# Optimization experiments

Measured on AMD Instinct MI355X. Metric: run time of the kernel, lower is better.

The kernel has to match this reference:

```python
import jax, jax.numpy as jnp
import numpy as np

B, S, E, H = 4, 2048, 1024, 16
D = E // H  # head dim = 64


def setup_inputs() -> dict:
    key = jax.random.key(0)
    ks = jax.random.split(key, 5)
    s = 0.02
    return {
        "x": jax.random.normal(ks[0], (B, S, E), dtype=jnp.float32),
        "Wq": jax.random.normal(ks[1], (E, E), dtype=jnp.float32) * s,
        "Wk": jax.random.normal(ks[2], (E, E), dtype=jnp.float32) * s,
        "Wv": jax.random.normal(ks[3], (E, E), dtype=jnp.float32) * s,
        "Wo": jax.random.normal(ks[4], (E, E), dtype=jnp.float32) * s,
        "bo": jnp.zeros((E,), dtype=jnp.float32),
    }


def reference(x, Wq, Wk, Wv, Wo, bo):
    b, s, e = x.shape
    h, d = H, e // H
    # QKV projections -> [b, h, s, d]
    q = (x @ Wq).reshape(b, s, h, d).transpose(0, 2, 1, 3)
    k = (x @ Wk).reshape(b, s, h, d).transpose(0, 2, 1, 3)
    v = (x @ Wv).reshape(b, s, h, d).transpose(0, 2, 1, 3)
    # scores [b, h, s, s], causal mask with -inf, scaled softmax
    a = jnp.einsum('bhqd,bhkd->bhqk', q, k)
    causal = jnp.tril(jnp.ones((s, s), dtype=bool))  # True where allowed
    a = jnp.where(causal, a, -jnp.inf) / jnp.sqrt(jnp.asarray(d, x.dtype))
    a = jax.nn.softmax(a, axis=-1)
    # dropout p=0.0 (identity in eval)
    y = jnp.einsum('bhqk,bhkd->bhqd', a, v)
    y = y.transpose(0, 2, 1, 3).reshape(b, s, e)
    return y @ Wo + bo
```

## Files before the change

kernel.cpp:

```cpp
#include <hip/hip_runtime.h>

typedef __bf16 bf16x8 __attribute__((ext_vector_type(8)));
typedef float f32x4 __attribute__((ext_vector_type(4)));
typedef unsigned short u16x8 __attribute__((ext_vector_type(8)));

#define S_LEN 2048
#define NHEAD 16
#define HDIM  64
#define EMB   1024

__device__ __forceinline__ ushort f2b(float v) {
  union { float f; unsigned u; } x; x.f = v;
  unsigned r = (x.u + 0x7fffu + ((x.u >> 16) & 1u)) >> 16;
  return (ushort)r;
}

__device__ __forceinline__ unsigned packtrunc(float a, float b) {
  union { float f; unsigned u; } x, y; x.f = a; y.f = b;
  return (x.u >> 16) | (y.u & 0xFFFF0000u);
}

typedef const __attribute__((address_space(1))) unsigned int* gp1_t;
typedef __attribute__((address_space(3))) unsigned int* lp3_t;
__device__ __forceinline__ void gld16(const ushort* g, const ushort* l) {
  __builtin_amdgcn_global_load_lds((gp1_t)(unsigned long long)(uintptr_t)g,
                                   (lp3_t)(unsigned int)(uintptr_t)l, 16, 0, 0);
}

__global__ __launch_bounds__(256) void prep_kernel(
    const float* __restrict__ x, const float* __restrict__ W0,
    const float* __restrict__ W1, const float* __restrict__ W2,
    const float* __restrict__ W3, ushort* __restrict__ xb,
    ushort* __restrict__ Wt0, ushort* __restrict__ Wt1,
    ushort* __restrict__ Wt2, ushort* __restrict__ Wt3, float scale0) {
  const int z = blockIdx.z;
  if (z == 4) {
    size_t base = ((size_t)(blockIdx.y * 32 + blockIdx.x)) * 8192 + threadIdx.x * 4;
#pragma unroll
    for (int i = 0; i < 8; ++i) {
      float4 v = *(const float4*)(x + base + i * 1024);
      ushort4 o;
      o.x = f2b(v.x); o.y = f2b(v.y); o.z = f2b(v.z); o.w = f2b(v.w);
      *(ushort4*)(xb + base + i * 1024) = o;
    }
    return;
  }
  __shared__ float t[32][33];
  const float* W = z == 0 ? W0 : (z == 1 ? W1 : (z == 2 ? W2 : W3));
  ushort* Wt = z == 0 ? Wt0 : (z == 1 ? Wt1 : (z == 2 ? Wt2 : Wt3));
  const float scale = z == 0 ? scale0 : 1.0f;
  int k0 = blockIdx.x * 32, n0 = blockIdx.y * 32;
  int c = threadIdx.x & 31, r0 = threadIdx.x >> 5;
#pragma unroll
  for (int i = 0; i < 4; ++i) {
    int r = r0 + i * 8;
    t[r][c] = W[(size_t)(k0 + r) * EMB + n0 + c];
  }
  __syncthreads();
#pragma unroll
  for (int i = 0; i < 4; ++i) {
    int r = r0 + i * 8;
    Wt[(size_t)(n0 + r) * EMB + k0 + c] = f2b(t[c][r] * scale);
  }
}

template <int EPI>
__global__ __launch_bounds__(256) void gemm_kernel(
    const ushort* __restrict__ A, const ushort* __restrict__ Bt, int K, int N,
    ushort* __restrict__ outQ, ushort* __restrict__ outK, ushort* __restrict__ outVt,
    float* __restrict__ outF, const float* __restrict__ bias) {
  __shared__ ushort As[2][128 * 32];
  __shared__ ushort Bs[2][128 * 32];
  const int tid = threadIdx.x;
  const int lane = tid & 63, ln = lane & 15, quad = lane >> 4;
  const int wave = tid >> 6, wm = wave >> 1, wn = wave & 1;
  const long m0 = (long)blockIdx.x * 128, n0 = (long)blockIdx.y * 128;

  const int sr = lane >> 2, sc = (lane & 3) * 8;
  const ushort* AgL = A + (m0 + 32 * wave + sr) * (long)K + sc;
  const ushort* BgL = Bt + (n0 + 32 * wave + sr) * (long)K + sc;

  f32x4 acc[4][4] = {};
  const int KT = K >> 5;

  {
    ushort* as = &As[0][32 * wave * 32];
    ushort* bs = &Bs[0][32 * wave * 32];
    gld16(AgL, as);
    gld16(AgL + 16 * (long)K, as + 16 * 32);
    gld16(BgL, bs);
    gld16(BgL + 16 * (long)K, bs + 16 * 32);
  }
  __syncthreads();

  for (int kt = 0; kt < KT; ++kt) {
    if (kt + 1 < KT) {
      const int nb = (kt + 1) & 1;
      const ushort* a = AgL + (kt + 1) * 32;
      const ushort* b = BgL + (kt + 1) * 32;
      ushort* as = &As[nb][32 * wave * 32];
      ushort* bs = &Bs[nb][32 * wave * 32];
      gld16(a, as);
      gld16(a + 16 * (long)K, as + 16 * 32);
      gld16(b, bs);
      gld16(b + 16 * (long)K, bs + 16 * 32);
    }
    const ushort* Ac = &As[kt & 1][0];
    const ushort* Bc = &Bs[kt & 1][0];
    bf16x8 af[4], bf[4];
#pragma unroll
    for (int mt = 0; mt < 4; ++mt)
      af[mt] = *(const bf16x8*)(Ac + (wm * 64 + mt * 16 + ln) * 32 + quad * 8);
#pragma unroll
    for (int nt = 0; nt < 4; ++nt)
      bf[nt] = *(const bf16x8*)(Bc + (wn * 64 + nt * 16 + ln) * 32 + quad * 8);
#pragma unroll
    for (int mt = 0; mt < 4; ++mt)
#pragma unroll
      for (int nt = 0; nt < 4; ++nt)
        acc[mt][nt] = __builtin_amdgcn_mfma_f32_16x16x32_bf16(af[mt], bf[nt], acc[mt][nt], 0, 0, 0);
    __syncthreads();
  }

  if (EPI == 0) {
    const int sel = (int)(n0 >> 10);
    if (sel == 2) {
#pragma unroll
      for (int mt = 0; mt < 4; ++mt) {
        const long mbase = m0 + wm * 64 + mt * 16 + quad * 4;
        const long bb = mbase >> 11, s = mbase & 2047;
#pragma unroll
        for (int nt = 0; nt < 4; ++nt) {
          const int nn = (int)((n0 & 1023) + wn * 64 + nt * 16 + ln);
          const int h = nn >> 6, d = nn & 63;
          uint2 val;
          val.x = (unsigned)f2b(acc[mt][nt][0]) | ((unsigned)f2b(acc[mt][nt][1]) << 16);
          val.y = (unsigned)f2b(acc[mt][nt][2]) | ((unsigned)f2b(acc[mt][nt][3]) << 16);
          *(uint2*)(outVt + (((bb * NHEAD + h) * (long)HDIM + d) * S_LEN) + s) = val;
        }
      }
    } else {
      ushort* dst = sel == 0 ? outQ : outK;
#pragma unroll
      for (int mt = 0; mt < 4; ++mt) {
#pragma unroll
        for (int nt = 0; nt < 4; ++nt) {
          const int nn = (int)((n0 & 1023) + wn * 64 + nt * 16 + ln);
          const int h = nn >> 6, d = nn & 63;
#pragma unroll
          for (int r = 0; r < 4; ++r) {
            const long m = m0 + wm * 64 + mt * 16 + quad * 4 + r;
            const long bb = m >> 11, s = m & 2047;
            dst[(((bb * NHEAD + h) * S_LEN) + s) * HDIM + d] = f2b(acc[mt][nt][r]);
          }
        }
      }
    }
  } else {
#pragma unroll
    for (int mt = 0; mt < 4; ++mt) {
#pragma unroll
      for (int nt = 0; nt < 4; ++nt) {
#pragma unroll
        for (int r = 0; r < 4; ++r) {
          const long m = m0 + wm * 64 + mt * 16 + quad * 4 + r;
          const long n = n0 + wn * 64 + nt * 16 + ln;
          outF[m * (long)N + n] = acc[mt][nt][r] + bias[n];
        }
      }
    }
  }
}

__global__ __launch_bounds__(256) void attn_kernel(const ushort* __restrict__ Q,
                                                   const ushort* __restrict__ Kg,
                                                   const ushort* __restrict__ Vt,
                                                   ushort* __restrict__ Y) {
  __shared__ alignas(16) ushort Ks[2][2 * 64 * 32];
  __shared__ alignas(16) ushort Vs[2][2 * 64 * 32];
  __shared__ alignas(16) ushort Ps[4 * 2 * 16 * 72];
  const int tid = threadIdx.x;
  const int wave = tid >> 6, lane = tid & 63, ln = lane & 15, quad = lane >> 4;
  const int bh = blockIdx.x;
  const int qb = 15 - (int)blockIdx.y;
  const int q0 = qb * 128;
  const size_t base = (size_t)bh * S_LEN * HDIM;
  const int ntiles = 2 * qb + 2;
  const int qbase = q0 + wave * 32;

  const u16x8 ob = {0x3F80, 0x3F80, 0x3F80, 0x3F80, 0x3F80, 0x3F80, 0x3F80, 0x3F80};
  const bf16x8 ones = __builtin_bit_cast(bf16x8, ob);

  bf16x8 qf[2][2];
#pragma unroll
  for (int mt = 0; mt < 2; ++mt)
#pragma unroll
    for (int ks2 = 0; ks2 < 2; ++ks2)
      qf[mt][ks2] = *(const bf16x8*)(Q + base + (size_t)(qbase + mt * 16 + ln) * HDIM +
                                     ks2 * 32 + quad * 8);

  f32x4 acc[2][4] = {};
  f32x4 accl[2] = {};

  const int sr = lane >> 2, sc = (lane & 3) * 8;
  const ushort* KgL = Kg + base + (size_t)(16 * wave + sr) * HDIM + sc;
  const ushort* VgL = Vt + base + (size_t)(16 * wave + sr) * S_LEN + sc;

  {
    ushort* kb = &Ks[0][16 * wave * 32];
    ushort* vb = &Vs[0][16 * wave * 32];
    gld16(KgL, kb);
    gld16(KgL + 32, kb + 2048);
    gld16(VgL, vb);
    gld16(VgL + 32, vb + 2048);
  }
  __syncthreads();

  ushort* Pw0 = Ps + wave * 2304;
  ushort* Pw1 = Pw0 + 1152;

  for (int kt = 0; kt < ntiles; ++kt) {
    const int cur = kt & 1;
    const int k0 = kt * 64;
    if (kt + 1 < ntiles) {
      const int nb = cur ^ 1;
      const size_t k1 = (size_t)(k0 + 64);
      ushort* kb = &Ks[nb][16 * wave * 32];
      ushort* vb = &Vs[nb][16 * wave * 32];
      gld16(KgL + k1 * HDIM, kb);
      gld16(KgL + k1 * HDIM + 32, kb + 2048);
      gld16(VgL + k1, vb);
      gld16(VgL + k1 + 32, vb + 2048);
    }
    const ushort* Kc = &Ks[cur][0];
    const ushort* Vc = &Vs[cur][0];

    if (k0 < qbase + 32) {
      f32x4 sT0[4] = {}, sT1[4] = {};
#pragma unroll
      for (int ks2 = 0; ks2 < 2; ++ks2) {
#pragma unroll
        for (int nt = 0; nt < 4; ++nt) {
          bf16x8 ak = *(const bf16x8*)(Kc + ks2 * 2048 + (nt * 16 + ln) * 32 + quad * 8);
          sT0[nt] = __builtin_amdgcn_mfma_f32_16x16x32_bf16(ak, qf[0][ks2], sT0[nt], 0, 0, 0);
          sT1[nt] = __builtin_amdgcn_mfma_f32_16x16x32_bf16(ak, qf[1][ks2], sT1[nt], 0, 0, 0);
        }
      }

      if (k0 + 63 > qbase) {
        const int thr0 = qbase + ln - k0 - quad * 4;
        const int thr1 = thr0 + 16;
#pragma unroll
        for (int nt = 0; nt < 4; ++nt)
#pragma unroll
          for (int r = 0; r < 4; ++r) {
            if (nt * 16 + r > thr0) sT0[nt][r] = -3.0e38f;
            if (nt * 16 + r > thr1) sT1[nt][r] = -3.0e38f;
          }
      }

      asm volatile("" ::: "memory");
#pragma unroll
      for (int nt = 0; nt < 4; ++nt) {
        uint2 w0, w1;
        w0.x = packtrunc(__builtin_amdgcn_exp2f(sT0[nt][0]), __builtin_amdgcn_exp2f(sT0[nt][1]));
        w0.y = packtrunc(__builtin_amdgcn_exp2f(sT0[nt][2]), __builtin_amdgcn_exp2f(sT0[nt][3]));
        w1.x = packtrunc(__builtin_amdgcn_exp2f(sT1[nt][0]), __builtin_amdgcn_exp2f(sT1[nt][1]));
        w1.y = packtrunc(__builtin_amdgcn_exp2f(sT1[nt][2]), __builtin_amdgcn_exp2f(sT1[nt][3]));
        const int off = ln * 72 + nt * 16 + quad * 4;
        *(uint2*)(Pw0 + off) = w0;
        *(uint2*)(Pw1 + off) = w1;
      }
      asm volatile("" ::: "memory");

#pragma unroll
      for (int ks2 = 0; ks2 < 2; ++ks2) {
        const int rcol = ks2 * 32 + quad * 8;
        bf16x8 ap0 = *(const bf16x8*)(Pw0 + ln * 72 + rcol);
        bf16x8 ap1 = *(const bf16x8*)(Pw1 + ln * 72 + rcol);
        accl[0] = __builtin_amdgcn_mfma_f32_16x16x32_bf16(ap0, ones, accl[0], 0, 0, 0);
        accl[1] = __builtin_amdgcn_mfma_f32_16x16x32_bf16(ap1, ones, accl[1], 0, 0, 0);
#pragma unroll
        for (int t2 = 0; t2 < 4; ++t2) {
          bf16x8 bv = *(const bf16x8*)(Vc + ks2 * 2048 + (t2 * 16 + ln) * 32 + quad * 8);
          acc[0][t2] = __builtin_amdgcn_mfma_f32_16x16x32_bf16(ap0, bv, acc[0][t2], 0, 0, 0);
          acc[1][t2] = __builtin_amdgcn_mfma_f32_16x16x32_bf16(ap1, bv, acc[1][t2], 0, 0, 0);
        }
      }
    }
    __syncthreads();
  }

  const long b = bh >> 4;
  const int h = bh & 15;
#pragma unroll
  for (int mt = 0; mt < 2; ++mt) {
#pragma unroll
    for (int r = 0; r < 4; ++r) {
      float inv = 1.0f / accl[mt][r];
      const int qq = qbase + mt * 16 + quad * 4 + r;
#pragma unroll
      for (int t2 = 0; t2 < 4; ++t2)
        Y[(((b * S_LEN + qq) * NHEAD) + h) * HDIM + t2 * 16 + ln] = f2b(acc[mt][t2][r] * inv);
    }
  }
}

extern "C" void kernel_launch(void* const* d_in, const int* in_sizes, int n_in,
                              void* d_out, int out_size, void* d_ws, size_t ws_size,
                              hipStream_t stream) {
  const float* x  = (const float*)d_in[0];
  const float* Wq = (const float*)d_in[1];
  const float* Wk = (const float*)d_in[2];
  const float* Wv = (const float*)d_in[3];
  const float* Wo = (const float*)d_in[4];
  const float* bo = (const float*)d_in[5];
  float* out = (float*)d_out;

  const size_t XE = (size_t)8192 * EMB;
  ushort* ws    = (ushort*)d_ws;
  ushort* xb    = ws;
  ushort* Wtqkv = xb + XE;
  ushort* Wto   = Wtqkv + 3 * 1048576;
  ushort* Qb    = Wto + 1048576;
  ushort* Kb    = Qb + XE;
  ushort* Vtb   = Kb + XE;
  ushort* Yb    = xb;

  const float SCALE_Q = 1.4426950408889634f / 8.0f;

  prep_kernel<<<dim3(32, 32, 5), 256, 0, stream>>>(
      x, Wq, Wk, Wv, Wo, xb, Wtqkv, Wtqkv + 1048576, Wtqkv + 2097152, Wto, SCALE_Q);

  gemm_kernel<0><<<dim3(64, 24), 256, 0, stream>>>(xb, Wtqkv, EMB, 3072,
                                                   Qb, Kb, Vtb, nullptr, nullptr);
  attn_kernel<<<dim3(64, 16), 256, 0, stream>>>(Qb, Kb, Vtb, Yb);
  gemm_kernel<1><<<dim3(64, 8), 256, 0, stream>>>(Yb, Wto, EMB, EMB,
                                                  nullptr, nullptr, nullptr, out, bo);
}
```

Measured before the change: 241.9 us.

## Double attention query tile per block to 256 rows for K/V reuse

Each attention block now handles 256 query rows (64 per wave, four 16-row sub-tiles) instead of 128, which halves the grid and doubles reuse of each staged K/V tile. K and V fragments are loaded into registers once per tile and shared across the four sub-tiles, and fully masked sub-tiles are skipped. Block order is rearranged so the heavy causal tiles are interleaved with light ones. The cost is more registers per wave (launch bounds set to 2 blocks), a larger P buffer in shared memory, and fewer blocks for load balancing.

```diff
diff --git a/kernel.cpp b/kernel.cpp
--- a/kernel.cpp
+++ b/kernel.cpp
@@ -172,35 +172,36 @@
   }
 }
 
-__global__ __launch_bounds__(256) void attn_kernel(const ushort* __restrict__ Q,
-                                                   const ushort* __restrict__ Kg,
-                                                   const ushort* __restrict__ Vt,
-                                                   ushort* __restrict__ Y) {
+__global__ __launch_bounds__(256, 2) void attn_kernel(const ushort* __restrict__ Q,
+                                                      const ushort* __restrict__ Kg,
+                                                      const ushort* __restrict__ Vt,
+                                                      ushort* __restrict__ Y) {
   __shared__ alignas(16) ushort Ks[2][2 * 64 * 32];
   __shared__ alignas(16) ushort Vs[2][2 * 64 * 32];
-  __shared__ alignas(16) ushort Ps[4 * 2 * 16 * 72];
+  __shared__ alignas(16) ushort Ps[4 * 4 * 16 * 72];
   const int tid = threadIdx.x;
   const int wave = tid >> 6, lane = tid & 63, ln = lane & 15, quad = lane >> 4;
   const int bh = blockIdx.x;
-  const int qb = 15 - (int)blockIdx.y;
-  const int q0 = qb * 128;
+  const int yb = (int)blockIdx.y;
+  const int qb = yb < 4 ? 7 - yb : yb - 4;
+  const int q0 = qb * 256;
   const size_t base = (size_t)bh * S_LEN * HDIM;
-  const int ntiles = 2 * qb + 2;
-  const int qbase = q0 + wave * 32;
+  const int ntiles = 4 * qb + 4;
+  const int qbase = q0 + wave * 64;
 
   const u16x8 ob = {0x3F80, 0x3F80, 0x3F80, 0x3F80, 0x3F80, 0x3F80, 0x3F80, 0x3F80};
   const bf16x8 ones = __builtin_bit_cast(bf16x8, ob);
 
-  bf16x8 qf[2][2];
-#pragma unroll
-  for (int mt = 0; mt < 2; ++mt)
+  bf16x8 qf[4][2];
+#pragma unroll
+  for (int h = 0; h < 4; ++h)
 #pragma unroll
     for (int ks2 = 0; ks2 < 2; ++ks2)
-      qf[mt][ks2] = *(const bf16x8*)(Q + base + (size_t)(qbase + mt * 16 + ln) * HDIM +
-                                     ks2 * 32 + quad * 8);
-
-  f32x4 acc[2][4] = {};
-  f32x4 accl[2] = {};
+      qf[h][ks2] = *(const bf16x8*)(Q + base + (size_t)(qbase + h * 16 + ln) * HDIM +
+                                    ks2 * 32 + quad * 8);
+
+  f32x4 acc[4][4] = {};
+  f32x4 accl[4] = {};
 
   const int sr = lane >> 2, sc = (lane & 3) * 8;
   const ushort* KgL = Kg + base + (size_t)(16 * wave + sr) * HDIM + sc;
@@ -216,8 +217,7 @@
   }
   __syncthreads();
 
-  ushort* Pw0 = Ps + wave * 2304;
-  ushort* Pw1 = Pw0 + 1152;
+  ushort* Pw = Ps + wave * 4608;
 
   for (int kt = 0; kt < ntiles; ++kt) {
     const int cur = kt & 1;
@@ -235,56 +235,61 @@
     const ushort* Kc = &Ks[cur][0];
     const ushort* Vc = &Vs[cur][0];
 
-    if (k0 < qbase + 32) {
-      f32x4 sT0[4] = {}, sT1[4] = {};
-#pragma unroll
-      for (int ks2 = 0; ks2 < 2; ++ks2) {
+    if (k0 < qbase + 64) {
+      bf16x8 ak[2][4];
+#pragma unroll
+      for (int ks2 = 0; ks2 < 2; ++ks2)
+#pragma unroll
+        for (int nt = 0; nt < 4; ++nt)
+          ak[ks2][nt] = *(const bf16x8*)(Kc + ks2 * 2048 + (nt * 16 + ln) * 32 + quad * 8);
+
+      asm volatile("" ::: "memory");
+#pragma unroll
+      for (int h = 0; h < 4; ++h) {
+        if (k0 > qbase + h * 16 + 15) continue;
+        f32x4 sT[4] = {};
+#pragma unroll
+        for (int ks2 = 0; ks2 < 2; ++ks2)
+#pragma unroll
+          for (int nt = 0; nt < 4; ++nt)
+            sT[nt] = __builtin_amdgcn_mfma_f32_16x16x32_bf16(ak[ks2][nt], qf[h][ks2], sT[nt], 0, 0, 0);
+
+        if (k0 + 63 > qbase + h * 16) {
+          const int thr = qbase + h * 16 + ln - k0 - quad * 4;
+#pragma unroll
+          for (int nt = 0; nt < 4; ++nt)
+#pragma unroll
+            for (int r = 0; r < 4; ++r)
+              if (nt * 16 + r > thr) sT[nt][r] = -3.0e38f;
+        }
+
 #pragma unroll
         for (int nt = 0; nt < 4; ++nt) {
-          bf16x8 ak = *(const bf16x8*)(Kc + ks2 * 2048 + (nt * 16 + ln) * 32 + quad * 8);
-          sT0[nt] = __builtin_amdgcn_mfma_f32_16x16x32_bf16(ak, qf[0][ks2], sT0[nt], 0, 0, 0);
-          sT1[nt] = __builtin_amdgcn_mfma_f32_16x16x32_bf16(ak, qf[1][ks2], sT1[nt], 0, 0, 0);
-        }
-      }
-
-      if (k0 + 63 > qbase) {
-        const int thr0 = qbase + ln - k0 - quad * 4;
-        const int thr1 = thr0 + 16;
-#pragma unroll
-        for (int nt = 0; nt < 4; ++nt)
-#pragma unroll
-          for (int r = 0; r < 4; ++r) {
-            if (nt * 16 + r > thr0) sT0[nt][r] = -3.0e38f;
-            if (nt * 16 + r > thr1) sT1[nt][r] = -3.0e38f;
-          }
-      }
-
+          uint2 w;
+          w.x = packtrunc(__builtin_amdgcn_exp2f(sT[nt][0]), __builtin_amdgcn_exp2f(sT[nt][1]));
+          w.y = packtrunc(__builtin_amdgcn_exp2f(sT[nt][2]), __builtin_amdgcn_exp2f(sT[nt][3]));
+          *(uint2*)(Pw + h * 1152 + ln * 72 + nt * 16 + quad * 4) = w;
+        }
+      }
       asm volatile("" ::: "memory");
-#pragma unroll
-      for (int nt = 0; nt < 4; ++nt) {
-        uint2 w0, w1;
-        w0.x = packtrunc(__builtin_amdgcn_exp2f(sT0[nt][0]), __builtin_amdgcn_exp2f(sT0[nt][1]));
-        w0.y = packtrunc(__builtin_amdgcn_exp2f(sT0[nt][2]), __builtin_amdgcn_exp2f(sT0[nt][3]));
-        w1.x = packtrunc(__builtin_amdgcn_exp2f(sT1[nt][0]), __builtin_amdgcn_exp2f(sT1[nt][1]));
-        w1.y = packtrunc(__builtin_amdgcn_exp2f(sT1[nt][2]), __builtin_amdgcn_exp2f(sT1[nt][3]));
-        const int off = ln * 72 + nt * 16 + quad * 4;
-        *(uint2*)(Pw0 + off) = w0;
-        *(uint2*)(Pw1 + off) = w1;
-      }
-      asm volatile("" ::: "memory");
-
-#pragma unroll
-      for (int ks2 = 0; ks2 < 2; ++ks2) {
-        const int rcol = ks2 * 32 + quad * 8;
-        bf16x8 ap0 = *(const bf16x8*)(Pw0 + ln * 72 + rcol);
-        bf16x8 ap1 = *(const bf16x8*)(Pw1 + ln * 72 + rcol);
-        accl[0] = __builtin_amdgcn_mfma_f32_16x16x32_bf16(ap0, ones, accl[0], 0, 0, 0);
-        accl[1] = __builtin_amdgcn_mfma_f32_16x16x32_bf16(ap1, ones, accl[1], 0, 0, 0);
-#pragma unroll
-        for (int t2 = 0; t2 < 4; ++t2) {
-          bf16x8 bv = *(const bf16x8*)(Vc + ks2 * 2048 + (t2 * 16 + ln) * 32 + quad * 8);
-          acc[0][t2] = __builtin_amdgcn_mfma_f32_16x16x32_bf16(ap0, bv, acc[0][t2], 0, 0, 0);
-          acc[1][t2] = __builtin_amdgcn_mfma_f32_16x16x32_bf16(ap1, bv, acc[1][t2], 0, 0, 0);
+
+      bf16x8 bv[2][4];
+#pragma unroll
+      for (int ks2 = 0; ks2 < 2; ++ks2)
+#pragma unroll
+        for (int t2 = 0; t2 < 4; ++t2)
+          bv[ks2][t2] = *(const bf16x8*)(Vc + ks2 * 2048 + (t2 * 16 + ln) * 32 + quad * 8);
+
+#pragma unroll
+      for (int h = 0; h < 4; ++h) {
+        if (k0 > qbase + h * 16 + 15) continue;
+#pragma unroll
+        for (int ks2 = 0; ks2 < 2; ++ks2) {
+          bf16x8 ap = *(const bf16x8*)(Pw + h * 1152 + ln * 72 + ks2 * 32 + quad * 8);
+          accl[h] = __builtin_amdgcn_mfma_f32_16x16x32_bf16(ap, ones, accl[h], 0, 0, 0);
+#pragma unroll
+          for (int t2 = 0; t2 < 4; ++t2)
+            acc[h][t2] = __builtin_amdgcn_mfma_f32_16x16x32_bf16(ap, bv[ks2][t2], acc[h][t2], 0, 0, 0);
         }
       }
     }
@@ -292,16 +297,16 @@
   }
 
   const long b = bh >> 4;
-  const int h = bh & 15;
-#pragma unroll
-  for (int mt = 0; mt < 2; ++mt) {
+  const int hh = bh & 15;
+#pragma unroll
+  for (int h = 0; h < 4; ++h) {
 #pragma unroll
     for (int r = 0; r < 4; ++r) {
-      float inv = 1.0f / accl[mt][r];
-      const int qq = qbase + mt * 16 + quad * 4 + r;
+      float inv = 1.0f / accl[h][r];
+      const int qq = qbase + h * 16 + quad * 4 + r;
 #pragma unroll
       for (int t2 = 0; t2 < 4; ++t2)
-        Y[(((b * S_LEN + qq) * NHEAD) + h) * HDIM + t2 * 16 + ln] = f2b(acc[mt][t2][r] * inv);
+        Y[(((b * S_LEN + qq) * NHEAD) + hh) * HDIM + t2 * 16 + ln] = f2b(acc[h][t2][r] * inv);
     }
   }
 }
@@ -334,7 +339,7 @@
 
   gemm_kernel<0><<<dim3(64, 24), 256, 0, stream>>>(xb, Wtqkv, EMB, 3072,
                                                    Qb, Kb, Vtb, nullptr, nullptr);
-  attn_kernel<<<dim3(64, 16), 256, 0, stream>>>(Qb, Kb, Vtb, Yb);
+  attn_kernel<<<dim3(64, 8), 256, 0, stream>>>(Qb, Kb, Vtb, Yb);
   gemm_kernel<1><<<dim3(64, 8), 256, 0, stream>>>(Yb, Wto, EMB, EMB,
                                                   nullptr, nullptr, nullptr, out, bo);
 }
```

After: 249.6 us. 1.03x slower.

## Fuse prep, QKV GEMM, attention and output GEMM into one persistent kernel

Applied to the files above, without the earlier changes.

Replaces four kernel launches with a single persistent kernel of 768 blocks that runs each stage in turn, separated by software grid barriers built on global atomics. Attention jobs are load-balanced by pairing causal query blocks, with short and long tiles combined on the extra 256 blocks. The goal is to remove launch gaps and tail effects between stages. In exchange it depends on all 768 blocks being co-resident (launch bounds of 3 blocks per CU), adds barrier spin overhead, and needs a memset before every launch.

```diff
diff --git a/kernel.cpp b/kernel.cpp
--- a/kernel.cpp
+++ b/kernel.cpp
@@ -8,6 +8,7 @@
 #define NHEAD 16
 #define HDIM  64
 #define EMB   1024
+#define NBLK  768
 
 __device__ __forceinline__ ushort f2b(float v) {
   union { float f; unsigned u; } x; x.f = v;
@@ -27,54 +28,40 @@
                                    (lp3_t)(unsigned int)(uintptr_t)l, 16, 0, 0);
 }
 
-__global__ __launch_bounds__(256) void prep_kernel(
-    const float* __restrict__ x, const float* __restrict__ W0,
-    const float* __restrict__ W1, const float* __restrict__ W2,
-    const float* __restrict__ W3, ushort* __restrict__ xb,
-    ushort* __restrict__ Wt0, ushort* __restrict__ Wt1,
-    ushort* __restrict__ Wt2, ushort* __restrict__ Wt3, float scale0) {
-  const int z = blockIdx.z;
-  if (z == 4) {
-    size_t base = ((size_t)(blockIdx.y * 32 + blockIdx.x)) * 8192 + threadIdx.x * 4;
-#pragma unroll
-    for (int i = 0; i < 8; ++i) {
-      float4 v = *(const float4*)(x + base + i * 1024);
-      ushort4 o;
-      o.x = f2b(v.x); o.y = f2b(v.y); o.z = f2b(v.z); o.w = f2b(v.w);
-      *(ushort4*)(xb + base + i * 1024) = o;
-    }
-    return;
-  }
-  __shared__ float t[32][33];
-  const float* W = z == 0 ? W0 : (z == 1 ? W1 : (z == 2 ? W2 : W3));
-  ushort* Wt = z == 0 ? Wt0 : (z == 1 ? Wt1 : (z == 2 ? Wt2 : Wt3));
-  const float scale = z == 0 ? scale0 : 1.0f;
-  int k0 = blockIdx.x * 32, n0 = blockIdx.y * 32;
-  int c = threadIdx.x & 31, r0 = threadIdx.x >> 5;
-#pragma unroll
-  for (int i = 0; i < 4; ++i) {
-    int r = r0 + i * 8;
-    t[r][c] = W[(size_t)(k0 + r) * EMB + n0 + c];
-  }
+__device__ __forceinline__ void gridbar(unsigned* bar) {
   __syncthreads();
-#pragma unroll
-  for (int i = 0; i < 4; ++i) {
-    int r = r0 + i * 8;
-    Wt[(size_t)(n0 + r) * EMB + k0 + c] = f2b(t[c][r] * scale);
-  }
-}
+  if (threadIdx.x == 0) {
+    __threadfence();
+    unsigned g = __hip_atomic_load(&bar[1], __ATOMIC_RELAXED, __HIP_MEMORY_SCOPE_AGENT);
+    unsigned a = __hip_atomic_fetch_add(&bar[0], 1u, __ATOMIC_ACQ_REL, __HIP_MEMORY_SCOPE_AGENT);
+    if (a == NBLK - 1) {
+      __hip_atomic_store(&bar[0], 0u, __ATOMIC_RELAXED, __HIP_MEMORY_SCOPE_AGENT);
+      __hip_atomic_store(&bar[1], g + 1u, __ATOMIC_RELEASE, __HIP_MEMORY_SCOPE_AGENT);
+    } else {
+      while (__hip_atomic_load(&bar[1], __ATOMIC_ACQUIRE, __HIP_MEMORY_SCOPE_AGENT) == g)
+        __builtin_amdgcn_s_sleep(8);
+    }
+    __threadfence();
+  }
+  __syncthreads();
+}
+
+union LdsU {
+  float wt[32][33];
+  struct { ushort A[2][4096]; ushort B[2][4096]; } g;
+  struct { ushort K[2][4096]; ushort V[2][4096]; ushort P[9216]; } a;
+};
 
 template <int EPI>
-__global__ __launch_bounds__(256) void gemm_kernel(
-    const ushort* __restrict__ A, const ushort* __restrict__ Bt, int K, int N,
-    ushort* __restrict__ outQ, ushort* __restrict__ outK, ushort* __restrict__ outVt,
-    float* __restrict__ outF, const float* __restrict__ bias) {
-  __shared__ ushort As[2][128 * 32];
-  __shared__ ushort Bs[2][128 * 32];
+__device__ __forceinline__ void gemm_tile(
+    int mi, int ni, const ushort* __restrict__ A, const ushort* __restrict__ Bt,
+    int K, int N, ushort* __restrict__ outQ, ushort* __restrict__ outK,
+    ushort* __restrict__ outVt, float* __restrict__ outF,
+    const float* __restrict__ bias, LdsU& lds) {
   const int tid = threadIdx.x;
   const int lane = tid & 63, ln = lane & 15, quad = lane >> 4;
   const int wave = tid >> 6, wm = wave >> 1, wn = wave & 1;
-  const long m0 = (long)blockIdx.x * 128, n0 = (long)blockIdx.y * 128;
+  const long m0 = (long)mi * 128, n0 = (long)ni * 128;
 
   const int sr = lane >> 2, sc = (lane & 3) * 8;
   const ushort* AgL = A + (m0 + 32 * wave + sr) * (long)K + sc;
@@ -84,8 +71,8 @@
   const int KT = K >> 5;
 
   {
-    ushort* as = &As[0][32 * wave * 32];
-    ushort* bs = &Bs[0][32 * wave * 32];
+    ushort* as = &lds.g.A[0][32 * wave * 32];
+    ushort* bs = &lds.g.B[0][32 * wave * 32];
     gld16(AgL, as);
     gld16(AgL + 16 * (long)K, as + 16 * 32);
     gld16(BgL, bs);
@@ -98,15 +85,15 @@
       const int nb = (kt + 1) & 1;
       const ushort* a = AgL + (kt + 1) * 32;
       const ushort* b = BgL + (kt + 1) * 32;
-      ushort* as = &As[nb][32 * wave * 32];
-      ushort* bs = &Bs[nb][32 * wave * 32];
+      ushort* as = &lds.g.A[nb][32 * wave * 32];
+      ushort* bs = &lds.g.B[nb][32 * wave * 32];
       gld16(a, as);
       gld16(a + 16 * (long)K, as + 16 * 32);
       gld16(b, bs);
       gld16(b + 16 * (long)K, bs + 16 * 32);
     }
-    const ushort* Ac = &As[kt & 1][0];
-    const ushort* Bc = &Bs[kt & 1][0];
+    const ushort* Ac = &lds.g.A[kt & 1][0];
+    const ushort* Bc = &lds.g.B[kt & 1][0];
     bf16x8 af[4], bf[4];
 #pragma unroll
     for (int mt = 0; mt < 4; ++mt)
@@ -123,7 +110,7 @@
   }
 
   if (EPI == 0) {
-    const int sel = (int)(n0 >> 10);
+    const int sel = ni >> 3;
     if (sel == 2) {
 #pragma unroll
       for (int mt = 0; mt < 4; ++mt) {
@@ -131,7 +118,7 @@
         const long bb = mbase >> 11, s = mbase & 2047;
 #pragma unroll
         for (int nt = 0; nt < 4; ++nt) {
-          const int nn = (int)((n0 & 1023) + wn * 64 + nt * 16 + ln);
+          const int nn = (int)(((n0 & 1023) + wn * 64 + nt * 16 + ln));
           const int h = nn >> 6, d = nn & 63;
           uint2 val;
           val.x = (unsigned)f2b(acc[mt][nt][0]) | ((unsigned)f2b(acc[mt][nt][1]) << 16);
@@ -145,7 +132,7 @@
       for (int mt = 0; mt < 4; ++mt) {
 #pragma unroll
         for (int nt = 0; nt < 4; ++nt) {
-          const int nn = (int)((n0 & 1023) + wn * 64 + nt * 16 + ln);
+          const int nn = (int)(((n0 & 1023) + wn * 64 + nt * 16 + ln));
           const int h = nn >> 6, d = nn & 63;
 #pragma unroll
           for (int r = 0; r < 4; ++r) {
@@ -172,17 +159,11 @@
   }
 }
 
-__global__ __launch_bounds__(256) void attn_kernel(const ushort* __restrict__ Q,
-                                                   const ushort* __restrict__ Kg,
-                                                   const ushort* __restrict__ Vt,
-                                                   ushort* __restrict__ Y) {
-  __shared__ alignas(16) ushort Ks[2][2 * 64 * 32];
-  __shared__ alignas(16) ushort Vs[2][2 * 64 * 32];
-  __shared__ alignas(16) ushort Ps[4 * 2 * 16 * 72];
+__device__ __forceinline__ void attn_job(
+    int bh, int qb, const ushort* __restrict__ Q, const ushort* __restrict__ Kg,
+    const ushort* __restrict__ Vt, ushort* __restrict__ Y, LdsU& lds) {
   const int tid = threadIdx.x;
   const int wave = tid >> 6, lane = tid & 63, ln = lane & 15, quad = lane >> 4;
-  const int bh = blockIdx.x;
-  const int qb = 15 - (int)blockIdx.y;
   const int q0 = qb * 128;
   const size_t base = (size_t)bh * S_LEN * HDIM;
   const int ntiles = 2 * qb + 2;
@@ -207,8 +188,8 @@
   const ushort* VgL = Vt + base + (size_t)(16 * wave + sr) * S_LEN + sc;
 
   {
-    ushort* kb = &Ks[0][16 * wave * 32];
-    ushort* vb = &Vs[0][16 * wave * 32];
+    ushort* kb = &lds.a.K[0][16 * wave * 32];
+    ushort* vb = &lds.a.V[0][16 * wave * 32];
     gld16(KgL, kb);
     gld16(KgL + 32, kb + 2048);
     gld16(VgL, vb);
@@ -216,7 +197,7 @@
   }
   __syncthreads();
 
-  ushort* Pw0 = Ps + wave * 2304;
+  ushort* Pw0 = lds.a.P + wave * 2304;
   ushort* Pw1 = Pw0 + 1152;
 
   for (int kt = 0; kt < ntiles; ++kt) {
@@ -225,15 +206,15 @@
     if (kt + 1 < ntiles) {
       const int nb = cur ^ 1;
       const size_t k1 = (size_t)(k0 + 64);
-      ushort* kb = &Ks[nb][16 * wave * 32];
-      ushort* vb = &Vs[nb][16 * wave * 32];
+      ushort* kb = &lds.a.K[nb][16 * wave * 32];
+      ushort* vb = &lds.a.V[nb][16 * wave * 32];
       gld16(KgL + k1 * HDIM, kb);
       gld16(KgL + k1 * HDIM + 32, kb + 2048);
       gld16(VgL + k1, vb);
       gld16(VgL + k1 + 32, vb + 2048);
     }
-    const ushort* Kc = &Ks[cur][0];
-    const ushort* Vc = &Vs[cur][0];
+    const ushort* Kc = &lds.a.K[cur][0];
+    const ushort* Vc = &lds.a.V[cur][0];
 
     if (k0 < qbase + 32) {
       f32x4 sT0[4] = {}, sT1[4] = {};
@@ -304,6 +285,75 @@
         Y[(((b * S_LEN + qq) * NHEAD) + h) * HDIM + t2 * 16 + ln] = f2b(acc[mt][t2][r] * inv);
     }
   }
+}
+
+__global__ __launch_bounds__(256, 3) void mega_kernel(
+    const float* __restrict__ x, const float* __restrict__ Wq,
+    const float* __restrict__ Wk, const float* __restrict__ Wv,
+    const float* __restrict__ Wo, const float* __restrict__ bo,
+    ushort* __restrict__ xb, ushort* __restrict__ Wtqkv, ushort* __restrict__ Wto,
+    ushort* __restrict__ Qb, ushort* __restrict__ Kb, ushort* __restrict__ Vtb,
+    float* __restrict__ out, unsigned* __restrict__ bar) {
+  __shared__ LdsU lds;
+  const int tid = threadIdx.x;
+  const int blk = (int)blockIdx.x;
+  const float SCALE_Q = 1.4426950408889634f / 8.0f;
+
+  if (blk < 512) {
+    size_t base0 = (size_t)blk * 16384 + tid * 4;
+#pragma unroll
+    for (int i = 0; i < 16; ++i) {
+      float4 v = *(const float4*)(x + base0 + i * 1024);
+      ushort4 o;
+      o.x = f2b(v.x); o.y = f2b(v.y); o.z = f2b(v.z); o.w = f2b(v.w);
+      *(ushort4*)(xb + base0 + i * 1024) = o;
+    }
+  }
+  for (int t = blk; t < 4096; t += NBLK) {
+    const int z = t >> 10, rem = t & 1023;
+    const int k0 = (rem & 31) * 32, n0 = (rem >> 5) * 32;
+    const float* W = z == 0 ? Wq : (z == 1 ? Wk : (z == 2 ? Wv : Wo));
+    ushort* Wt = z == 0 ? Wtqkv : (z == 1 ? Wtqkv + 1048576 : (z == 2 ? Wtqkv + 2097152 : Wto));
+    const float scale = z == 0 ? SCALE_Q : 1.0f;
+    const int c = tid & 31, r0 = tid >> 5;
+    __syncthreads();
+#pragma unroll
+    for (int i = 0; i < 4; ++i) {
+      int r = r0 + i * 8;
+      lds.wt[r][c] = W[(size_t)(k0 + r) * EMB + n0 + c];
+    }
+    __syncthreads();
+#pragma unroll
+    for (int i = 0; i < 4; ++i) {
+      int r = r0 + i * 8;
+      Wt[(size_t)(n0 + r) * EMB + k0 + c] = f2b(lds.wt[c][r] * scale);
+    }
+  }
+  gridbar(bar);
+
+  {
+    int idx = blk;
+    gemm_tile<0>(idx & 63, idx >> 6, xb, Wtqkv, EMB, 3072, Qb, Kb, Vtb, nullptr, nullptr, lds);
+    idx = blk + NBLK;
+    gemm_tile<0>(idx & 63, idx >> 6, xb, Wtqkv, EMB, 3072, Qb, Kb, Vtb, nullptr, nullptr, lds);
+  }
+  gridbar(bar);
+
+  {
+    ushort* Yb = xb;
+    if (blk < 512) {
+      attn_job(blk & 63, 15 - (blk >> 6), Qb, Kb, Vtb, Yb, lds);
+    } else {
+      const int b2 = blk - 512, s = b2 >> 6;
+      attn_job(b2 & 63, 7 - s, Qb, Kb, Vtb, Yb, lds);
+      attn_job(b2 & 63, s, Qb, Kb, Vtb, Yb, lds);
+    }
+  }
+  gridbar(bar);
+
+  if (blk < 512)
+    gemm_tile<1>(blk & 63, blk >> 6, xb , Wto, EMB, EMB,
+                 nullptr, nullptr, nullptr, out, bo, lds);
 }
 
 extern "C" void kernel_launch(void* const* d_in, const int* in_sizes, int n_in,
@@ -325,16 +375,9 @@
   ushort* Qb    = Wto + 1048576;
   ushort* Kb    = Qb + XE;
   ushort* Vtb   = Kb + XE;
-  ushort* Yb    = xb;
-
-  const float SCALE_Q = 1.4426950408889634f / 8.0f;
-
-  prep_kernel<<<dim3(32, 32, 5), 256, 0, stream>>>(
-      x, Wq, Wk, Wv, Wo, xb, Wtqkv, Wtqkv + 1048576, Wtqkv + 2097152, Wto, SCALE_Q);
-
-  gemm_kernel<0><<<dim3(64, 24), 256, 0, stream>>>(xb, Wtqkv, EMB, 3072,
-                                                   Qb, Kb, Vtb, nullptr, nullptr);
-  attn_kernel<<<dim3(64, 16), 256, 0, stream>>>(Qb, Kb, Vtb, Yb);
-  gemm_kernel<1><<<dim3(64, 8), 256, 0, stream>>>(Yb, Wto, EMB, EMB,
-                                                  nullptr, nullptr, nullptr, out, bo);
-}
+  unsigned* bar = (unsigned*)(Vtb + XE);
+
+  hipMemsetAsync(bar, 0, 16, stream);
+  mega_kernel<<<NBLK, 256, 0, stream>>>(x, Wq, Wk, Wv, Wo, bo,
+                                        xb, Wtqkv, Wto, Qb, Kb, Vtb, out, bar);
+}
```

New measurement: 697.7 us. 188% more time.
